# Kernel optimization log

Hardware: AMD Instinct MI355X
Metric: run time of the kernel (lower is better)

The kernel has to match this reference:

```python
import jax, jax.numpy as jnp
import numpy as np

B, S, DX, DH = 8, 4096, 1024, 1024

def setup_inputs() -> dict:
    key = jax.random.key(0)
    ks = jax.random.split(key, 7)
    s_x = 1.0 / np.sqrt(DX)
    s_h = 1.0 / np.sqrt(DH)
    return {
        "x":  jax.random.normal(ks[0], (B, S, DX), dtype=jnp.float32),
        "Wz": jax.random.uniform(ks[1], (DH, DX), jnp.float32, -s_x, s_x),
        "bz": jax.random.uniform(ks[2], (DH,),   jnp.float32, -s_x, s_x),
        "Wh": jax.random.uniform(ks[3], (DH, DX), jnp.float32, -s_x, s_x),
        "bh": jax.random.uniform(ks[4], (DH,),   jnp.float32, -s_x, s_x),
        "Wo": jax.random.uniform(ks[5], (DX, DH), jnp.float32, -s_h, s_h),
        "bo": jax.random.uniform(ks[6], (DX,),   jnp.float32, -s_h, s_h),
    }

def log_g(x):
    # Appendix B.3 of "Were RNNs All We Needed?"
    return jnp.where(x >= 0, jnp.log(jax.nn.relu(x) + 0.5), -jax.nn.softplus(-x))

def parallel_scan_log(log_coeffs, log_values):
    # Heinsen log-space associative scan: h_t = a_t * h_{t-1} + b_t (h_0 = 0)
    a_star = jnp.cumsum(log_coeffs, axis=1)                       # [B,S,H]
    log_h = a_star + jax.lax.cumlogsumexp(log_values - a_star, axis=1)
    return jnp.exp(log_h)

def reference(x, Wz, bz, Wh, bh, Wo, bo):
    k       = jnp.einsum('bsd,hd->bsh', x, Wz) + bz               # pre-gate
    tilde_h = jnp.einsum('bsd,hd->bsh', x, Wh) + bh               # candidate
    log_z           = -jax.nn.softplus(-k)                        # log sigmoid(k)
    log_one_minus_z = -jax.nn.softplus(k)                         # log sigmoid(-k)
    log_tilde_h     = log_g(tilde_h)
    h = parallel_scan_log(log_one_minus_z, log_z + log_tilde_h)   # [B,S,H]
    out = jnp.einsum('bsh,dh->bsd', h, Wo) + bo                   # [B,S,DX]
    return out
```

## Files before the change

### kernel.cpp

```cpp
#include <hip/hip_runtime.h>
#include <stdint.h>
#include <stddef.h>


typedef __bf16 bf16;
typedef __bf16 bf16x8 __attribute__((ext_vector_type(8)));
typedef float f32x4 __attribute__((ext_vector_type(4)));

#define DEV __device__ __forceinline__

DEV void gload_lds16(const bf16* g, bf16* l) {
  __builtin_amdgcn_global_load_lds((const __attribute__((address_space(1))) void*)g,
                                   (__attribute__((address_space(3))) void*)l,
                                   16, 0, 0);
}

DEV void xcd_tiles(int bx, int by, int gx_lg, int& tileM, int& tileN) {
  const int d = (by << gx_lg) + bx;
  const int xcd = d & 7;
  const int i = d >> 3;
  tileM = (xcd * 32 + (i >> gx_lg)) * 128;
  tileN = (i & ((1 << gx_lg) - 1)) * 128;
}

DEV void chk_sample(int w, int& m, int& n) {
  if (w < 64)       { m = w;              n = (w * 97) & 1023; }
  else if (w < 128) { m = 32767 - (w - 64); n = (w * 97) & 1023; }
  else              { m = (w * 12347) & 32767; n = (w * 4099) & 1023; }
}

__global__ __launch_bounds__(256)
void conv_b(const float* __restrict__ src, bf16* __restrict__ dst, int n4) {
  const int stride = gridDim.x * 256;
  for (int i = blockIdx.x * 256 + threadIdx.x; i < n4; i += stride) {
    float4 v = ((const float4*)src)[i];
    bf16 o[4] = {(bf16)v.x, (bf16)v.y, (bf16)v.z, (bf16)v.w};
    *(uint64_t*)(dst + 4 * (size_t)i) = *(uint64_t*)o;
  }
}

__global__ __launch_bounds__(256)
void conv_w3(const float* __restrict__ wz, const float* __restrict__ wh,
             const float* __restrict__ wo,
             bf16* __restrict__ w2, bf16* __restrict__ wob) {
  const int stride = gridDim.x * 256;
  for (int i = blockIdx.x * 256 + threadIdx.x; i < 786432; i += stride) {
    if (i < 262144) {
      const int j = i, n = j >> 8, c = j & 255;
      float4 v = ((const float4*)wz)[j];
      bf16 o[4] = {(bf16)v.x, (bf16)v.y, (bf16)v.z, (bf16)v.w};
      *(uint64_t*)(w2 + 4 * ((size_t)(n << 9) + c)) = *(uint64_t*)o;
    } else if (i < 524288) {
      const int j = i - 262144, n = j >> 8, c = j & 255;
      float4 v = ((const float4*)wh)[j];
      bf16 o[4] = {(bf16)v.x, (bf16)v.y, (bf16)v.z, (bf16)v.w};
      *(uint64_t*)(w2 + 4 * ((size_t)(n << 9) + 256 + c)) = *(uint64_t*)o;
    } else {
      const int j = i - 524288;
      float4 v = ((const float4*)wo)[j];
      bf16 o[4] = {(bf16)v.x, (bf16)v.y, (bf16)v.z, (bf16)v.w};
      *(uint64_t*)(wob + 4 * (size_t)j) = *(uint64_t*)o;
    }
  }
}

__global__ __launch_bounds__(256, 3)
void gate_gemm(const bf16* __restrict__ X, const bf16* __restrict__ W2,
               const float* __restrict__ bzf, const float* __restrict__ bhf,
               bf16* __restrict__ avB) {
  __shared__ __align__(16) bf16 SMEM[17408];
  bf16* As = SMEM;
  bf16* Bs = SMEM + 8192;

  const int lane = threadIdx.x & 63;
  const int wave = threadIdx.x >> 6;
  const int wm = wave >> 1, wn = wave & 1;
  int tileM, tileN;
  xcd_tiles(blockIdx.x, blockIdx.y, 4, tileM, tileN);
  const int q = lane >> 4, r = lane & 15;
  const int srow = lane >> 2;
  const int scol = (lane & 3) * 8;

  const bf16* ga[2]; const bf16* gb[2]; bf16* la[2]; bf16* lb[2];
#pragma unroll
  for (int j = 0; j < 2; ++j) {
    const int cid = j * 4 + wave;
    const int row = cid * 16 + srow;
    ga[j] = X  + (size_t)(tileM + row) * 1024 + scol;
    gb[j] = W2 + (size_t)(tileN + row) * 1024 + scol;
    la[j] = As + cid * 512;
    lb[j] = Bs + cid * 512;
  }
  const bf16* pA[4]; const bf16* pB[4];
#pragma unroll
  for (int f = 0; f < 4; ++f) {
    pA[f] = As + (wm * 64 + f * 16 + r) * 32 + q * 8;
    pB[f] = Bs + (wn * 64 + f * 16 + r) * 32 + q * 8;
  }

  f32x4 acc[4][4];
#pragma unroll
  for (int i = 0; i < 4; ++i)
#pragma unroll
    for (int j = 0; j < 4; ++j) acc[i][j] = (f32x4){0.f, 0.f, 0.f, 0.f};

  auto STAGE = [&](int buf, int k0) {
    const int bo = buf * 4096;
#pragma unroll
    for (int j = 0; j < 2; ++j) {
      gload_lds16(ga[j] + k0, la[j] + bo);
      gload_lds16(gb[j] + k0, lb[j] + bo);
    }
  };
  auto COMPUTE = [&](int buf) {
    const int bo = buf * 4096;
    bf16x8 af[4];
#pragma unroll
    for (int fm = 0; fm < 4; ++fm) af[fm] = *(const bf16x8*)(pA[fm] + bo);
#pragma unroll
    for (int fn = 0; fn < 4; ++fn) {
      bf16x8 b8 = *(const bf16x8*)(pB[fn] + bo);
#pragma unroll
      for (int fm = 0; fm < 4; ++fm)
        acc[fm][fn] = __builtin_amdgcn_mfma_f32_16x16x32_bf16(af[fm], b8, acc[fm][fn], 0, 0, 0);
    }
  };

  STAGE(0, 0);
  int cur = 0;
  for (int t = 0; t < 31; ++t) {
    __syncthreads();
    STAGE(cur ^ 1, (t + 1) * 32);
    COMPUTE(cur);
    cur ^= 1;
  }
  __syncthreads();
  COMPUTE(cur);

  __syncthreads();
  bf16* C = SMEM;
#pragma unroll
  for (int fn = 0; fn < 4; ++fn) {
    const int cl = wn * 64 + fn * 16 + r;
    const int n = (tileN + cl) >> 1;
    const float bz = bzf[n], bh = bhf[n];
#pragma unroll
    for (int fm = 0; fm < 4; ++fm) {
      const int ml = wm * 64 + fm * 16 + q * 4;
#pragma unroll
      for (int i = 0; i < 4; ++i) {
        const float val = acc[fm][fn][i];
        const float oth = __shfl_xor(val, 1);
        const float kraw  = (lane & 1) ? oth : val;
        const float thraw = (lane & 1) ? val : oth;
        const float k  = kraw + bz;
        const float th = thraw + bh;
        const float e   = __expf(-k);
        const float inv = 1.f / (1.f + e);
        const float a   = e * inv;
        const float g   = (th >= 0.f) ? (th + 0.5f)
                                      : (1.f / (1.f + __expf(-th)));
        const float res = (lane & 1) ? (inv * g) : a;
        C[(ml + i) * 136 + cl] = (bf16)res;
      }
    }
  }
  __syncthreads();
  const int tT = threadIdx.x;
#pragma unroll
  for (int p = 0; p < 8; ++p) {
    const int row  = p * 16 + (tT >> 4);
    const int col8 = (tT & 15) * 8;
    bf16x8 v8 = *(const bf16x8*)(C + row * 136 + col8);
    *(bf16x8*)(avB + (size_t)(tileM + row) * 2048 + tileN + col8) = v8;
  }
}

__global__ __launch_bounds__(256)
void chk_gate(const float* __restrict__ Xf,
              const float* __restrict__ Wzf, const float* __restrict__ Whf,
              const float* __restrict__ bzf, const float* __restrict__ bhf,
              const bf16* __restrict__ avB, int* __restrict__ badA) {
  const int w = (blockIdx.x * 256 + threadIdx.x) >> 6;
  const int lane = threadIdx.x & 63;
  int m, n;
  chk_sample(w, m, n);
  float kz = 0.f, kh = 0.f;
  for (int k = lane; k < 1024; k += 64) {
    float xv = Xf[(size_t)m * 1024 + k];
    kz = fmaf(xv, Wzf[(size_t)n * 1024 + k], kz);
    kh = fmaf(xv, Whf[(size_t)n * 1024 + k], kh);
  }
#pragma unroll
  for (int off = 32; off; off >>= 1) {
    kz += __shfl_xor(kz, off);
    kh += __shfl_xor(kh, off);
  }
  if (lane == 0) {
    kz += bzf[n]; kh += bhf[n];
    float e = __expf(-kz), inv = 1.f / (1.f + e);
    float a = e * inv;
    float g = (kh >= 0.f) ? (kh + 0.5f) : (1.f / (1.f + __expf(-kh)));
    float v = inv * g;
    size_t idx = (size_t)m * 2048 + 2 * n;
    int ok = (fabsf((float)avB[idx] - a) <= 0.04f) &&
             (fabsf((float)avB[idx + 1] - v) <= 0.08f);
    if (!ok) atomicAdd(badA, 1);
  }
}

__global__ __launch_bounds__(256)
void fb_gate(const int* __restrict__ badA, const float* __restrict__ Xf,
             const float* __restrict__ Wzf, const float* __restrict__ Whf,
             const float* __restrict__ bzf, const float* __restrict__ bhf,
             bf16* __restrict__ avB) {
  if (*badA < 4) return;
  const int n = (blockIdx.x & 3) * 256 + threadIdx.x;
  const int m0 = (blockIdx.x >> 2) * 16;
  for (int mi = 0; mi < 16; ++mi) {
    const int m = m0 + mi;
    float kz = 0.f, kh = 0.f;
    for (int k = 0; k < 1024; ++k) {
      float xv = Xf[(size_t)m * 1024 + k];
      kz = fmaf(xv, Wzf[(size_t)n * 1024 + k], kz);
      kh = fmaf(xv, Whf[(size_t)n * 1024 + k], kh);
    }
    kz += bzf[n]; kh += bhf[n];
    float e = __expf(-kz), inv = 1.f / (1.f + e);
    float a = e * inv;
    float g = (kh >= 0.f) ? (kh + 0.5f) : (1.f / (1.f + __expf(-kh)));
    size_t idx = (size_t)m * 2048 + 2 * n;
    avB[idx] = (bf16)a;
    avB[idx + 1] = (bf16)(inv * g);
  }
}

__global__ __launch_bounds__(256)
void scan_phase1(const bf16* __restrict__ avB,
                 float* __restrict__ Ac, float* __restrict__ Vc) {
  const int tid = blockIdx.x * 256 + threadIdx.x;
  const int hg = tid & 127, c = (tid >> 7) & 63, b = tid >> 13;
  const size_t base = (size_t)(b * 4096 + c * 64) * 2048 + hg * 16;
  float A[8], V[8];
#pragma unroll
  for (int j = 0; j < 8; ++j) { A[j] = 1.f; V[j] = 0.f; }
#pragma unroll 8
  for (int t = 0; t < 64; ++t) {
    bf16 arr[16];
    *(bf16x8*)(arr)     = *(const bf16x8*)(avB + base + (size_t)t * 2048);
    *(bf16x8*)(arr + 8) = *(const bf16x8*)(avB + base + (size_t)t * 2048 + 8);
#pragma unroll
    for (int j = 0; j < 8; ++j) {
      float a = (float)arr[2 * j];
      V[j] = fmaf(a, V[j], (float)arr[2 * j + 1]);
      A[j] *= a;
    }
  }
  const size_t o = (size_t)(b * 64 + c) * 1024 + hg * 8;
#pragma unroll
  for (int j = 0; j < 8; ++j) { Ac[o + j] = A[j]; Vc[o + j] = V[j]; }
}

__global__ __launch_bounds__(256)
void scan_phase2(const float* __restrict__ Ac, const float* __restrict__ Vc,
                 float* __restrict__ Hin) {
  const int tid = blockIdx.x * 256 + threadIdx.x;
  const int h = tid & 1023, b = tid >> 10;
  float carry = 0.f;
  for (int c = 0; c < 64; ++c) {
    const int idx = (b * 64 + c) * 1024 + h;
    Hin[idx] = carry;
    carry = fmaf(Ac[idx], carry, Vc[idx]);
  }
}

__global__ __launch_bounds__(256)
void scan_phase3(const bf16* __restrict__ avB, const float* __restrict__ Hin,
                 bf16* __restrict__ hB) {
  const int tid = blockIdx.x * 256 + threadIdx.x;
  const int hg = tid & 127, c = (tid >> 7) & 63, b = tid >> 13;
  const size_t base = (size_t)(b * 4096 + c * 64) * 2048 + hg * 16;
  const size_t bout = (size_t)(b * 4096 + c * 64) * 1024 + hg * 8;
  const size_t o = (size_t)(b * 64 + c) * 1024 + hg * 8;
  float hc[8];
#pragma unroll
  for (int j = 0; j < 8; ++j) hc[j] = Hin[o + j];
#pragma unroll 4
  for (int t = 0; t < 64; ++t) {
    bf16 arr[16];
    *(bf16x8*)(arr)     = *(const bf16x8*)(avB + base + (size_t)t * 2048);
    *(bf16x8*)(arr + 8) = *(const bf16x8*)(avB + base + (size_t)t * 2048 + 8);
    bf16x8 h8;
#pragma unroll
    for (int j = 0; j < 8; ++j) {
      hc[j] = fmaf((float)arr[2 * j], hc[j], (float)arr[2 * j + 1]);
      h8[j] = (bf16)hc[j];
    }
    *(bf16x8*)(hB + bout + (size_t)t * 1024) = h8;
  }
}

__global__ __launch_bounds__(256, 3)
void out_gemm(const bf16* __restrict__ H, const bf16* __restrict__ Wo,
              const float* __restrict__ bof, float* __restrict__ O) {
  __shared__ __align__(16) bf16 As[2 * 4096];
  __shared__ __align__(16) bf16 Bs[2 * 4096];

  const int lane = threadIdx.x & 63;
  const int wave = threadIdx.x >> 6;
  const int wm = wave >> 1, wn = wave & 1;
  int tileM, tileN;
  xcd_tiles(blockIdx.x, blockIdx.y, 3, tileM, tileN);
  const int q = lane >> 4, r = lane & 15;
  const int srow = lane >> 2;
  const int scol = (lane & 3) * 8;

  const bf16* ga[2]; const bf16* gb[2]; bf16* la[2]; bf16* lb[2];
#pragma unroll
  for (int j = 0; j < 2; ++j) {
    const int cid = j * 4 + wave;
    const int row = cid * 16 + srow;
    ga[j] = H  + (size_t)(tileM + row) * 1024 + scol;
    gb[j] = Wo + (size_t)(tileN + row) * 1024 + scol;
    la[j] = As + cid * 512;
    lb[j] = Bs + cid * 512;
  }
  const bf16* pA[4]; const bf16* pB[4];
#pragma unroll
  for (int f = 0; f < 4; ++f) {
    pA[f] = As + (wm * 64 + f * 16 + r) * 32 + q * 8;
    pB[f] = Bs + (wn * 64 + f * 16 + r) * 32 + q * 8;
  }

  f32x4 acc[4][4];
#pragma unroll
  for (int i = 0; i < 4; ++i)
#pragma unroll
    for (int j = 0; j < 4; ++j) acc[i][j] = (f32x4){0.f, 0.f, 0.f, 0.f};

  auto STAGE = [&](int buf, int k0) {
    const int bo = buf * 4096;
#pragma unroll
    for (int j = 0; j < 2; ++j) {
      gload_lds16(ga[j] + k0, la[j] + bo);
      gload_lds16(gb[j] + k0, lb[j] + bo);
    }
  };
  auto COMPUTE = [&](int buf) {
    const int bo = buf * 4096;
    bf16x8 af[4];
#pragma unroll
    for (int fm = 0; fm < 4; ++fm) af[fm] = *(const bf16x8*)(pA[fm] + bo);
#pragma unroll
    for (int fn = 0; fn < 4; ++fn) {
      bf16x8 b8 = *(const bf16x8*)(pB[fn] + bo);
#pragma unroll
      for (int fm = 0; fm < 4; ++fm)
        acc[fm][fn] = __builtin_amdgcn_mfma_f32_16x16x32_bf16(af[fm], b8, acc[fm][fn], 0, 0, 0);
    }
  };

  STAGE(0, 0);
  int cur = 0;
  for (int t = 0; t < 31; ++t) {
    __syncthreads();
    STAGE(cur ^ 1, (t + 1) * 32);
    COMPUTE(cur);
    cur ^= 1;
  }
  __syncthreads();
  COMPUTE(cur);

#pragma unroll
  for (int fn = 0; fn < 4; ++fn) {
    const int n = tileN + wn * 64 + fn * 16 + r;
    const float bov = bof[n];
#pragma unroll
    for (int fm = 0; fm < 4; ++fm) {
      const int m0 = tileM + wm * 64 + fm * 16 + q * 4;
#pragma unroll
      for (int i = 0; i < 4; ++i)
        O[(size_t)(m0 + i) * 1024 + n] = acc[fm][fn][i] + bov;
    }
  }
}

__global__ __launch_bounds__(256)
void chk_out(const bf16* __restrict__ H, const float* __restrict__ Wof,
             const float* __restrict__ bof, const float* __restrict__ O,
             int* __restrict__ badB) {
  const int w = (blockIdx.x * 256 + threadIdx.x) >> 6;
  const int lane = threadIdx.x & 63;
  int m, n;
  chk_sample(w, m, n);
  float acc = 0.f;
  for (int k = lane; k < 1024; k += 64)
    acc = fmaf((float)H[(size_t)m * 1024 + k], Wof[(size_t)n * 1024 + k], acc);
#pragma unroll
  for (int off = 32; off; off >>= 1) acc += __shfl_xor(acc, off);
  if (lane == 0) {
    acc += bof[n];
    int ok = fabsf(O[(size_t)m * 1024 + n] - acc) <= 0.05f;
    if (!ok) atomicAdd(badB, 1);
  }
}

__global__ __launch_bounds__(256)
void fb_out(const int* __restrict__ badB, const bf16* __restrict__ H,
            const float* __restrict__ Wof, const float* __restrict__ bof,
            float* __restrict__ O) {
  if (*badB < 4) return;
  const int n = (blockIdx.x & 3) * 256 + threadIdx.x;
  const int m0 = (blockIdx.x >> 2) * 16;
  for (int mi = 0; mi < 16; ++mi) {
    const int m = m0 + mi;
    float acc = 0.f;
    for (int k = 0; k < 1024; ++k)
      acc = fmaf((float)H[(size_t)m * 1024 + k], Wof[(size_t)n * 1024 + k], acc);
    O[(size_t)m * 1024 + n] = acc + bof[n];
  }
}

extern "C" void kernel_launch(void* const* d_in, const int* in_sizes, int n_in,
                              void* d_out, int out_size, void* d_ws, size_t ws_size,
                              hipStream_t stream) {
  char* ws = (char*)d_ws;
  bf16*  avB = (bf16*)(ws);
  float* Ac  = (float*)(ws + 134217728ull);
  float* Vc  = (float*)(ws + 136314880ull);
  float* Hin = (float*)(ws + 138412032ull);
  int*   flags = (int*)(ws + 140509184ull);
  bf16*  w2b = (bf16*)(ws + 140525568ull);
  bf16*  wob = (bf16*)(ws + 144719872ull);
  bf16*  xb  = (bf16*)(ws + 146817024ull);

  const float* Xf  = (const float*)d_in[0];
  const float* Wzf = (const float*)d_in[1];
  const float* bzf = (const float*)d_in[2];
  const float* Whf = (const float*)d_in[3];
  const float* bhf = (const float*)d_in[4];
  const float* Wof = (const float*)d_in[5];
  const float* bof = (const float*)d_in[6];

  hipMemsetAsync(flags, 0, 8, stream);
  conv_b<<<4096, 256, 0, stream>>>(Xf, xb, 8388608);
  conv_w3<<<3072, 256, 0, stream>>>(Wzf, Whf, Wof, w2b, wob);

  dim3 blk(256);
  dim3 gg(16, 256);
  dim3 go(8, 256);

  gate_gemm<<<gg, blk, 0, stream>>>(xb, w2b, bzf, bhf, avB);
  chk_gate<<<256, blk, 0, stream>>>(Xf, Wzf, Whf, bzf, bhf, avB, flags);
  fb_gate<<<8192, blk, 0, stream>>>(flags, Xf, Wzf, Whf, bzf, bhf, avB);

  scan_phase1<<<256, blk, 0, stream>>>(avB, Ac, Vc);
  scan_phase2<<<32,  blk, 0, stream>>>(Ac, Vc, Hin);
  scan_phase3<<<256, blk, 0, stream>>>(avB, Hin, xb );

  out_gemm<<<go, blk, 0, stream>>>(xb, wob, bof, (float*)d_out);
  chk_out<<<256, blk, 0, stream>>>(xb, Wof, bof, (const float*)d_out, flags + 1);
  fb_out<<<8192, blk, 0, stream>>>(flags + 1, xb, Wof, bof, (float*)d_out);
}
```

Baseline: 605.3 us.

## Fuse scan chunk reduction into gate GEMM epilogue, swizzle LDS, use fast rcp

The gate GEMM epilogue now computes each 64-step chunk's scan aggregate (A product, V value) from the shared-memory tile and writes Ac/Vc directly. The standalone phase-1 scan kernel only runs as a fallback when the gate check flags errors. Both GEMMs also XOR-swizzle their LDS layout to reduce bank conflicts, and the sigmoid math uses v_rcp_f32 with a branch-free select. This removes one full pass over the gate buffer, at the cost of a slightly less precise reciprocal and an epilogue in which only half the threads do the serial chunk scan.

```diff
diff --git a/kernel.cpp b/kernel.cpp
--- a/kernel.cpp
+++ b/kernel.cpp
@@ -13,6 +13,12 @@
   __builtin_amdgcn_global_load_lds((const __attribute__((address_space(1))) void*)g,
                                    (__attribute__((address_space(3))) void*)l,
                                    16, 0, 0);
+}
+
+DEV float fast_rcp(float x) {
+  float r;
+  asm("v_rcp_f32 %0, %1" : "=v"(r) : "v"(x));
+  return r;
 }
 
 DEV void xcd_tiles(int bx, int by, int gx_lg, int& tileM, int& tileN) {
@@ -24,8 +30,8 @@
 }
 
 DEV void chk_sample(int w, int& m, int& n) {
-  if (w < 64)       { m = w;              n = (w * 97) & 1023; }
-  else if (w < 128) { m = 32767 - (w - 64); n = (w * 97) & 1023; }
+  if (w < 64)       { m = w;                 n = (w * 97) & 1023; }
+  else if (w < 128) { m = 32767 - (w - 64);  n = (w * 97) & 1023; }
   else              { m = (w * 12347) & 32767; n = (w * 4099) & 1023; }
 }
 
@@ -67,7 +73,8 @@
 __global__ __launch_bounds__(256, 3)
 void gate_gemm(const bf16* __restrict__ X, const bf16* __restrict__ W2,
                const float* __restrict__ bzf, const float* __restrict__ bhf,
-               bf16* __restrict__ avB) {
+               bf16* __restrict__ avB,
+               float* __restrict__ Ac, float* __restrict__ Vc) {
   __shared__ __align__(16) bf16 SMEM[17408];
   bf16* As = SMEM;
   bf16* Bs = SMEM + 8192;
@@ -79,7 +86,7 @@
   xcd_tiles(blockIdx.x, blockIdx.y, 4, tileM, tileN);
   const int q = lane >> 4, r = lane & 15;
   const int srow = lane >> 2;
-  const int scol = (lane & 3) * 8;
+  const int scol = (((lane & 3) ^ ((lane >> 3) & 3)) * 8);
 
   const bf16* ga[2]; const bf16* gb[2]; bf16* la[2]; bf16* lb[2];
 #pragma unroll
@@ -91,11 +98,12 @@
     la[j] = As + cid * 512;
     lb[j] = Bs + cid * 512;
   }
+  const int q2 = q ^ ((r >> 1) & 3);
   const bf16* pA[4]; const bf16* pB[4];
 #pragma unroll
   for (int f = 0; f < 4; ++f) {
-    pA[f] = As + (wm * 64 + f * 16 + r) * 32 + q * 8;
-    pB[f] = Bs + (wn * 64 + f * 16 + r) * 32 + q * 8;
+    pA[f] = As + (wm * 64 + f * 16 + r) * 32 + q2 * 8;
+    pB[f] = Bs + (wn * 64 + f * 16 + r) * 32 + q2 * 8;
   }
 
   f32x4 acc[4][4];
@@ -151,15 +159,14 @@
       for (int i = 0; i < 4; ++i) {
         const float val = acc[fm][fn][i];
         const float oth = __shfl_xor(val, 1);
-        const float kraw  = (lane & 1) ? oth : val;
-        const float thraw = (lane & 1) ? val : oth;
-        const float k  = kraw + bz;
-        const float th = thraw + bh;
-        const float e   = __expf(-k);
-        const float inv = 1.f / (1.f + e);
+        const float kv = ((lane & 1) ? oth : val) + bz;
+        const float th = ((lane & 1) ? val : oth) + bh;
+        const float e   = __expf(-kv);
+        const float inv = fast_rcp(1.f + e);
         const float a   = e * inv;
-        const float g   = (th >= 0.f) ? (th + 0.5f)
-                                      : (1.f / (1.f + __expf(-th)));
+        const float eh  = __expf(-th);
+        const float sg  = fast_rcp(1.f + eh);
+        const float g   = (th >= 0.f) ? (th + 0.5f) : sg;
         const float res = (lane & 1) ? (inv * g) : a;
         C[(ml + i) * 136 + cl] = (bf16)res;
       }
@@ -173,6 +180,23 @@
     const int col8 = (tT & 15) * 8;
     bf16x8 v8 = *(const bf16x8*)(C + row * 136 + col8);
     *(bf16x8*)(avB + (size_t)(tileM + row) * 2048 + tileN + col8) = v8;
+  }
+  if (tT < 128) {
+    const int ch = tT >> 6, u = tT & 63;
+    const bf16* Cp = C + (ch * 64) * 136 + u * 2;
+    float A = 1.f, V = 0.f;
+#pragma unroll 8
+    for (int t = 0; t < 64; ++t) {
+      union { uint32_t u32; bf16 h[2]; } cv;
+      cv.u32 = *(const uint32_t*)(Cp + t * 136);
+      const float a = (float)cv.h[0], v = (float)cv.h[1];
+      V = fmaf(a, V, v);
+      A *= a;
+    }
+    const int b  = tileM >> 12;
+    const int c0 = (tileM & 4095) >> 6;
+    const size_t o = (size_t)(b * 64 + c0 + ch) * 1024 + (tileN >> 1) + u;
+    Ac[o] = A; Vc[o] = V;
   }
 }
 
@@ -236,15 +260,15 @@
 }
 
 __global__ __launch_bounds__(256)
-void scan_phase1(const bf16* __restrict__ avB,
-                 float* __restrict__ Ac, float* __restrict__ Vc) {
+void scan_phase1_fb(const int* __restrict__ badA, const bf16* __restrict__ avB,
+                    float* __restrict__ Ac, float* __restrict__ Vc) {
+  if (*badA < 4) return;
   const int tid = blockIdx.x * 256 + threadIdx.x;
   const int hg = tid & 127, c = (tid >> 7) & 63, b = tid >> 13;
   const size_t base = (size_t)(b * 4096 + c * 64) * 2048 + hg * 16;
   float A[8], V[8];
 #pragma unroll
   for (int j = 0; j < 8; ++j) { A[j] = 1.f; V[j] = 0.f; }
-#pragma unroll 8
   for (int t = 0; t < 64; ++t) {
     bf16 arr[16];
     *(bf16x8*)(arr)     = *(const bf16x8*)(avB + base + (size_t)t * 2048);
@@ -313,7 +337,7 @@
   xcd_tiles(blockIdx.x, blockIdx.y, 3, tileM, tileN);
   const int q = lane >> 4, r = lane & 15;
   const int srow = lane >> 2;
-  const int scol = (lane & 3) * 8;
+  const int scol = (((lane & 3) ^ ((lane >> 3) & 3)) * 8);
 
   const bf16* ga[2]; const bf16* gb[2]; bf16* la[2]; bf16* lb[2];
 #pragma unroll
@@ -325,11 +349,12 @@
     la[j] = As + cid * 512;
     lb[j] = Bs + cid * 512;
   }
+  const int q2 = q ^ ((r >> 1) & 3);
   const bf16* pA[4]; const bf16* pB[4];
 #pragma unroll
   for (int f = 0; f < 4; ++f) {
-    pA[f] = As + (wm * 64 + f * 16 + r) * 32 + q * 8;
-    pB[f] = Bs + (wn * 64 + f * 16 + r) * 32 + q * 8;
+    pA[f] = As + (wm * 64 + f * 16 + r) * 32 + q2 * 8;
+    pB[f] = Bs + (wn * 64 + f * 16 + r) * 32 + q2 * 8;
   }
 
   f32x4 acc[4][4];
@@ -450,11 +475,11 @@
   dim3 gg(16, 256);
   dim3 go(8, 256);
 
-  gate_gemm<<<gg, blk, 0, stream>>>(xb, w2b, bzf, bhf, avB);
+  gate_gemm<<<gg, blk, 0, stream>>>(xb, w2b, bzf, bhf, avB, Ac, Vc);
   chk_gate<<<256, blk, 0, stream>>>(Xf, Wzf, Whf, bzf, bhf, avB, flags);
   fb_gate<<<8192, blk, 0, stream>>>(flags, Xf, Wzf, Whf, bzf, bhf, avB);
-
-  scan_phase1<<<256, blk, 0, stream>>>(avB, Ac, Vc);
+  scan_phase1_fb<<<256, blk, 0, stream>>>(flags, avB, Ac, Vc);
+
   scan_phase2<<<32,  blk, 0, stream>>>(Ac, Vc, Hin);
   scan_phase3<<<256, blk, 0, stream>>>(avB, Hin, xb );
 
```

Result: faster. 568.7 us (-6.1%).
